# Kernel tuning notes

Measured on AMD Instinct MI355X. Metric: run time of the kernel, lower is better.

## Reference

```python
import jax, jax.numpy as jnp
import numpy as np

E, C, H, I = 8, 1024, 2048, 4096  # experts, capacity, hidden, intermediate


def setup_inputs() -> dict:
    key = jax.random.key(0)
    k1, k2, k3 = jax.random.split(key, 3)
    hidden_states = jax.random.normal(k1, (E, C, H), dtype=jnp.float32)
    # fused gate/up projection weights per expert: [E, H, 2*I]
    w_gate_up = jax.random.normal(k2, (E, H, 2 * I), dtype=jnp.float32) * (1.0 / np.sqrt(H))
    # down projection weights per expert: [E, I, H]
    w_down = jax.random.normal(k3, (E, I, H), dtype=jnp.float32) * (1.0 / np.sqrt(I))
    return {"hidden_states": hidden_states, "w_gate_up": w_gate_up, "w_down": w_down}


def reference(hidden_states, w_gate_up, w_down):
    # Batched per-expert gate/up GEMM: (E,C,H) @ (E,H,2I) -> (E,C,2I)
    gate_up = jnp.einsum("ech,ehf->ecf", hidden_states, w_gate_up)
    gate, up = jnp.split(gate_up, 2, axis=-1)  # each (E,C,I)
    act = jax.nn.silu(gate) * up  # GLU activation
    # Batched per-expert down GEMM: (E,C,I) @ (E,I,H) -> (E,C,H)
    out = jnp.einsum("eci,eih->ech", act, w_down)
    return out
```

## Files before the change

### kernel.cpp

```cpp
#include <hip/hip_runtime.h>
#include <stdint.h>


#define E_  8
#define C_  1024
#define H_  2048
#define I_  4096
#define N1_ 8192

typedef __bf16 bf16x8 __attribute__((ext_vector_type(8)));
typedef float  f32x4  __attribute__((ext_vector_type(4)));

typedef __attribute__((address_space(3))) unsigned       lds_uint;
typedef const __attribute__((address_space(1))) unsigned glob_uint;

__device__ __forceinline__ void gload_lds16(const void* g, void* l) {
    __builtin_amdgcn_global_load_lds((glob_uint*)g, (lds_uint*)l, 16, 0, 0);
}

__device__ __forceinline__ unsigned short f2bf(float f) {
    union { float f; unsigned u; } v; v.f = f;
    unsigned u = v.u;
    return (unsigned short)((u + 0x7FFFu + ((u >> 16) & 1u)) >> 16);
}

__device__ __forceinline__ unsigned swz8(unsigned row) {
    return ((row ^ (row >> 2)) & 7u) << 4;
}

#define SBAR0 __builtin_amdgcn_sched_barrier(0)
#define MFMA_ __builtin_amdgcn_mfma_f32_16x16x32_bf16

__global__ void k_convert(const float* __restrict__ src,
                          unsigned short* __restrict__ dst, int n8) {
    int idx = blockIdx.x * blockDim.x + threadIdx.x;
    int stride = gridDim.x * blockDim.x;
    for (int i = idx; i < n8; i += stride) {
        const float4* s = reinterpret_cast<const float4*>(src + (size_t)i * 8);
        float4 a = s[0], b = s[1];
        ushort4 lo, hi;
        lo.x = f2bf(a.x); lo.y = f2bf(a.y); lo.z = f2bf(a.z); lo.w = f2bf(a.w);
        hi.x = f2bf(b.x); hi.y = f2bf(b.y); hi.z = f2bf(b.z); hi.w = f2bf(b.w);
        ushort4* d = reinterpret_cast<ushort4*>(dst + (size_t)i * 8);
        d[0] = lo; d[1] = hi;
    }
}

template<int LD>
__device__ __forceinline__ void stageA(const char* __restrict__ gtile,
                                       char* ldst, int j, int tid, int wave) {
    unsigned p   = (unsigned)(j * 8192 + tid * 16);
    unsigned row = p >> 7;
    unsigned kb  = (p & 127u) ^ swz8(row);
    const char* gp = gtile + (size_t)row * LD + kb;
    void* lp = ldst + j * 8192 + wave * 1024;
    gload_lds16(gp, lp);
}

__device__ __forceinline__ const bf16x8* frag128(const char* tile, int row, int kb) {
    unsigned phys = (unsigned)(row * 128) + ((unsigned)kb ^ swz8((unsigned)row));
    return reinterpret_cast<const bf16x8*>(tile + phys);
}

template<int LDB>
__device__ __forceinline__ void loadB8(const char* __restrict__ gcol, int kt,
                                       float4 (&bk)[8]) {
    const char* p = gcol + (size_t)(kt * 64) * LDB;
    #pragma unroll
    for (int i = 0; i < 8; ++i)
        bk[i] = *reinterpret_cast<const float4*>(p + (size_t)i * LDB);
}

__device__ __forceinline__ void cvtWriteB(char* bB, const float4 (&bk)[8],
                                          int rg, int kg8) {
    const float* f = reinterpret_cast<const float*>(&bk[0]);
    #pragma unroll
    for (int j = 0; j < 4; ++j) {
        unsigned u[4];
        #pragma unroll
        for (int p2 = 0; p2 < 4; ++p2) {
            float lo = f[(2 * p2) * 4 + j];
            float hi = f[(2 * p2 + 1) * 4 + j];
            asm("v_cvt_pk_bf16_f32 %0, %1, %2" : "=v"(u[p2]) : "v"(lo), "v"(hi));
        }
        unsigned q = (unsigned)(rg * 4 + j);
        unsigned phys = q * 128 + (((unsigned)kg8 * 16) ^ swz8(q));
        *reinterpret_cast<uint4*>(bB + phys) = make_uint4(u[0], u[1], u[2], u[3]);
    }
}

template<int LDA, int LDB, int NT, int BMG, int BNG, int MODE>
__global__ __launch_bounds__(512, 2) void k_gemm_f(
    const unsigned short* __restrict__ A,
    const float* __restrict__ B,
    void* __restrict__ Cout,
    size_t sA, size_t sB) {
    __shared__ char lds[131072];

    const int tid = threadIdx.x, lane = tid & 63, wave = tid >> 6;
    const int wm = wave >> 2, wn = wave & 3;
    const int kg = lane >> 4, r = lane & 15;
    const int rg = tid & 63, kg8 = tid >> 6;

    unsigned flat = blockIdx.x;
    unsigned cpx = gridDim.x >> 3;
    unsigned nid = (flat & 7u) * cpx + (flat >> 3);
    const int bm = nid % BMG;
    const int bn = (nid / BMG) % BNG;
    const int e  = nid / (BMG * BNG);

    const char* gA = (const char*)(A + sA * e) + (size_t)(bm * 256) * LDA;
    size_t colstart;
    if constexpr (MODE == 0)
        colstart = (size_t)(bn * 128 + ((rg >> 4) & 3) * 32 + ((rg >> 2) & 1) * 16
                            + (rg & 3) * 4)
                 + (((rg >> 3) & 1) ? (size_t)I_ : (size_t)0);
    else
        colstart = (size_t)(bn * 256 + rg * 4);
    const char* gBcol = (const char*)B + sB * e + colstart * 4
                      + (size_t)kg8 * 8 * LDB;

    float4 bk[8];

    loadB8<LDB>(gBcol, 0, bk);
    SBAR0;
    asm volatile("s_waitcnt vmcnt(0)" ::: "memory");
    SBAR0;
    cvtWriteB(lds + 32768, bk, rg, kg8);
    SBAR0;
    stageA<LDA>(gA, lds, 0, tid, wave);
    stageA<LDA>(gA, lds, 1, tid, wave);
    stageA<LDA>(gA, lds, 2, tid, wave);
    stageA<LDA>(gA, lds, 3, tid, wave);
    SBAR0;
    loadB8<LDB>(gBcol, 1, bk);
    SBAR0;
    asm volatile("s_waitcnt vmcnt(8)" ::: "memory");
    asm volatile("s_waitcnt lgkmcnt(0)" ::: "memory");
    SBAR0;
    __builtin_amdgcn_s_barrier();
    SBAR0;

    f32x4 acc[8][4] = {};

    for (int t = 0; t < NT; ++t) {
        const char* Ab = lds + (t & 1) * 65536;
        const char* Bb = Ab + 32768;
        char* nA = lds + ((t + 1) & 1) * 65536;
        char* nB = nA + 32768;
        const char* gAn = gA + (size_t)(t + 1) * 128;
        const bool hs1 = (t + 1) < NT, hs2 = (t + 2) < NT;

        bf16x8 af[8], b0[2], bg[2];

        if (hs1) {
            asm volatile("s_waitcnt vmcnt(0)" ::: "memory");
            SBAR0;
            cvtWriteB(nB, bk, rg, kg8);
            SBAR0;
            stageA<LDA>(gAn, nA, 0, tid, wave);
            stageA<LDA>(gAn, nA, 1, tid, wave);
            stageA<LDA>(gAn, nA, 2, tid, wave);
            stageA<LDA>(gAn, nA, 3, tid, wave);
            SBAR0;
            if (hs2) { loadB8<LDB>(gBcol, t + 2, bk); SBAR0; }
        }

        #pragma unroll
        for (int m = 0; m < 8; ++m)
            af[m] = *frag128(Ab, wm * 128 + m * 16 + r, kg * 16);
        #pragma unroll
        for (int n = 0; n < 2; ++n)
            b0[n] = *frag128(Bb, wn * 64 + n * 16 + r, kg * 16);
        __builtin_amdgcn_s_setprio(1);
        #pragma unroll
        for (int m = 0; m < 8; ++m) {
            acc[m][0] = MFMA_(af[m], b0[0], acc[m][0], 0, 0, 0);
            acc[m][1] = MFMA_(af[m], b0[1], acc[m][1], 0, 0, 0);
        }
        __builtin_amdgcn_s_setprio(0);

        #pragma unroll
        for (int n = 0; n < 2; ++n)
            bg[n] = *frag128(Bb, wn * 64 + 32 + n * 16 + r, kg * 16);
        __builtin_amdgcn_s_setprio(1);
        #pragma unroll
        for (int m = 0; m < 8; ++m) {
            acc[m][2] = MFMA_(af[m], bg[0], acc[m][2], 0, 0, 0);
            acc[m][3] = MFMA_(af[m], bg[1], acc[m][3], 0, 0, 0);
        }
        __builtin_amdgcn_s_setprio(0);

        #pragma unroll
        for (int m = 0; m < 8; ++m)
            af[m] = *frag128(Ab, wm * 128 + m * 16 + r, 64 + kg * 16);
        #pragma unroll
        for (int n = 0; n < 2; ++n)
            b0[n] = *frag128(Bb, wn * 64 + n * 16 + r, 64 + kg * 16);
        __builtin_amdgcn_s_setprio(1);
        #pragma unroll
        for (int m = 0; m < 8; ++m) {
            acc[m][0] = MFMA_(af[m], b0[0], acc[m][0], 0, 0, 0);
            acc[m][1] = MFMA_(af[m], b0[1], acc[m][1], 0, 0, 0);
        }
        __builtin_amdgcn_s_setprio(0);

        #pragma unroll
        for (int n = 0; n < 2; ++n)
            bg[n] = *frag128(Bb, wn * 64 + 32 + n * 16 + r, 64 + kg * 16);
        __builtin_amdgcn_s_setprio(1);
        #pragma unroll
        for (int m = 0; m < 8; ++m) {
            acc[m][2] = MFMA_(af[m], bg[0], acc[m][2], 0, 0, 0);
            acc[m][3] = MFMA_(af[m], bg[1], acc[m][3], 0, 0, 0);
        }
        __builtin_amdgcn_s_setprio(0);

        if (hs1) {
            SBAR0;
            if (hs2) asm volatile("s_waitcnt vmcnt(8)" ::: "memory");
            else     asm volatile("s_waitcnt vmcnt(0)" ::: "memory");
            asm volatile("s_waitcnt lgkmcnt(0)" ::: "memory");
            SBAR0;
            __builtin_amdgcn_s_barrier();
            SBAR0;
        }
    }

    const int row0 = bm * 256 + wm * 128 + kg * 4;
    if constexpr (MODE == 0) {
        unsigned short* act = (unsigned short*)Cout + (size_t)e * C_ * I_;
        const int col0 = bn * 128 + wn * 32 + r;
        #pragma unroll
        for (int m = 0; m < 8; ++m)
            #pragma unroll
            for (int n = 0; n < 2; ++n)
                #pragma unroll
                for (int j = 0; j < 4; ++j) {
                    float g = acc[m][n][j], u = acc[m][n + 2][j];
                    float s = g / (1.0f + __expf(-g)) * u;
                    act[(size_t)(row0 + m * 16 + j) * I_ + col0 + n * 16] = f2bf(s);
                }
    } else {
        float* o = (float*)Cout + (size_t)e * C_ * H_;
        const int col0 = bn * 256 + wn * 64 + r;
        #pragma unroll
        for (int m = 0; m < 8; ++m)
            #pragma unroll
            for (int n = 0; n < 4; ++n)
                #pragma unroll
                for (int j = 0; j < 4; ++j)
                    o[(size_t)(row0 + m * 16 + j) * H_ + col0 + n * 16] = acc[m][n][j];
    }
}

extern "C" void kernel_launch(void* const* d_in, const int* in_sizes, int n_in,
                              void* d_out, int out_size, void* d_ws, size_t ws_size,
                              hipStream_t stream) {
    const float* hs  = (const float*)d_in[0];
    const float* wgu = (const float*)d_in[1];
    const float* wd  = (const float*)d_in[2];
    float* out = (float*)d_out;

    char* ws = (char*)d_ws;
    unsigned short* Xbf  = (unsigned short*)(ws);
    unsigned short* actb = (unsigned short*)(ws + 33554432ull);

    k_convert<<<2048, 256, 0, stream>>>(hs, Xbf, E_ * C_ * H_ / 8);

    k_gemm_f<H_ * 2, N1_ * 4, H_ / 64, 4, 32, 0><<<dim3(1024), 512, 0, stream>>>(
        Xbf, wgu, actb, (size_t)C_ * H_, (size_t)H_ * N1_ * 4);

    k_gemm_f<I_ * 2, H_ * 4, I_ / 64, 4, 8, 1><<<dim3(256), 512, 0, stream>>>(
        actb, wd, out, (size_t)C_ * I_, (size_t)I_ * H_ * 4);
}
```

Baseline: 470.7 us.

## Use 1024-thread blocks with 4x4 per-wave MFMA tiles and new LDS swizzle

Doubles the workgroup to 16 waves over the same 256x128/256x256 block tile, so each wave computes a 64x64 sub-tile (4x4 MFMAs) instead of 128x64. The B loader now fetches float2 per thread and writes two rows, and the LDS XOR swizzle gains an extra term. The aim is more waves to hide latency and fewer registers per thread, at the cost of more LDS fragment reads per MFMA and heavier barrier synchronisation. The launch_bounds(1024,4) request is unlikely to be met with 128KB of LDS per block.

New measurement: 788.8 us. 1.68x slower.

```diff
diff --git a/kernel.cpp b/kernel.cpp
--- a/kernel.cpp
+++ b/kernel.cpp
@@ -24,8 +24,8 @@
     return (unsigned short)((u + 0x7FFFu + ((u >> 16) & 1u)) >> 16);
 }
 
-__device__ __forceinline__ unsigned swz8(unsigned row) {
-    return ((row ^ (row >> 2)) & 7u) << 4;
+__device__ __forceinline__ unsigned swzf(unsigned q) {
+    return ((q ^ (q >> 1) ^ (q >> 2)) & 7u) << 4;
 }
 
 #define SBAR0 __builtin_amdgcn_sched_barrier(0)
@@ -49,48 +49,47 @@
 template<int LD>
 __device__ __forceinline__ void stageA(const char* __restrict__ gtile,
                                        char* ldst, int j, int tid, int wave) {
-    unsigned p   = (unsigned)(j * 8192 + tid * 16);
+    unsigned p   = (unsigned)(j * 16384 + tid * 16);
     unsigned row = p >> 7;
-    unsigned kb  = (p & 127u) ^ swz8(row);
+    unsigned kb  = (p & 127u) ^ swzf(row);
     const char* gp = gtile + (size_t)row * LD + kb;
-    void* lp = ldst + j * 8192 + wave * 1024;
+    void* lp = ldst + j * 16384 + wave * 1024;
     gload_lds16(gp, lp);
 }
 
 __device__ __forceinline__ const bf16x8* frag128(const char* tile, int row, int kb) {
-    unsigned phys = (unsigned)(row * 128) + ((unsigned)kb ^ swz8((unsigned)row));
+    unsigned phys = (unsigned)(row * 128) + ((unsigned)kb ^ swzf((unsigned)row));
     return reinterpret_cast<const bf16x8*>(tile + phys);
 }
 
 template<int LDB>
-__device__ __forceinline__ void loadB8(const char* __restrict__ gcol, int kt,
-                                       float4 (&bk)[8]) {
-    const char* p = gcol + (size_t)(kt * 64) * LDB;
+__device__ __forceinline__ void loadB8(const float* __restrict__ gcol, int kt,
+                                       float2 (&bk)[8]) {
+    const float* p = gcol + (size_t)(kt * 64) * LDB;
     #pragma unroll
     for (int i = 0; i < 8; ++i)
-        bk[i] = *reinterpret_cast<const float4*>(p + (size_t)i * LDB);
-}
-
-__device__ __forceinline__ void cvtWriteB(char* bB, const float4 (&bk)[8],
-                                          int rg, int kg8) {
-    const float* f = reinterpret_cast<const float*>(&bk[0]);
+        bk[i] = *reinterpret_cast<const float2*>(p + (size_t)i * LDB);
+}
+
+__device__ __forceinline__ void cvtWriteB(char* bB, const float2 (&bk)[8],
+                                          int rg, int ko) {
     #pragma unroll
-    for (int j = 0; j < 4; ++j) {
+    for (int cc = 0; cc < 2; ++cc) {
         unsigned u[4];
         #pragma unroll
         for (int p2 = 0; p2 < 4; ++p2) {
-            float lo = f[(2 * p2) * 4 + j];
-            float hi = f[(2 * p2 + 1) * 4 + j];
+            float lo = cc ? bk[2 * p2].y     : bk[2 * p2].x;
+            float hi = cc ? bk[2 * p2 + 1].y : bk[2 * p2 + 1].x;
             asm("v_cvt_pk_bf16_f32 %0, %1, %2" : "=v"(u[p2]) : "v"(lo), "v"(hi));
         }
-        unsigned q = (unsigned)(rg * 4 + j);
-        unsigned phys = q * 128 + (((unsigned)kg8 * 16) ^ swz8(q));
+        unsigned q = (unsigned)(2 * rg + cc);
+        unsigned phys = q * 128 + (((unsigned)ko * 16) ^ swzf(q));
         *reinterpret_cast<uint4*>(bB + phys) = make_uint4(u[0], u[1], u[2], u[3]);
     }
 }
 
 template<int LDA, int LDB, int NT, int BMG, int BNG, int MODE>
-__global__ __launch_bounds__(512, 2) void k_gemm_f(
+__global__ __launch_bounds__(1024, 4) void k_gemm_f(
     const unsigned short* __restrict__ A,
     const float* __restrict__ B,
     void* __restrict__ Cout,
@@ -100,7 +99,7 @@
     const int tid = threadIdx.x, lane = tid & 63, wave = tid >> 6;
     const int wm = wave >> 2, wn = wave & 3;
     const int kg = lane >> 4, r = lane & 15;
-    const int rg = tid & 63, kg8 = tid >> 6;
+    const int rg = tid & 127, ko = tid >> 7;
 
     unsigned flat = blockIdx.x;
     unsigned cpx = gridDim.x >> 3;
@@ -112,26 +111,22 @@
     const char* gA = (const char*)(A + sA * e) + (size_t)(bm * 256) * LDA;
     size_t colstart;
     if constexpr (MODE == 0)
-        colstart = (size_t)(bn * 128 + ((rg >> 4) & 3) * 32 + ((rg >> 2) & 1) * 16
-                            + (rg & 3) * 4)
+        colstart = (size_t)(bn * 128 + ((rg >> 4) * 16) + 2 * (rg & 7))
                  + (((rg >> 3) & 1) ? (size_t)I_ : (size_t)0);
     else
-        colstart = (size_t)(bn * 256 + rg * 4);
-    const char* gBcol = (const char*)B + sB * e + colstart * 4
-                      + (size_t)kg8 * 8 * LDB;
-
-    float4 bk[8];
+        colstart = (size_t)(bn * 256 + 2 * rg);
+    const float* gBcol = B + sB * e + colstart + (size_t)ko * 8 * LDB;
+
+    float2 bk[8];
 
     loadB8<LDB>(gBcol, 0, bk);
     SBAR0;
     asm volatile("s_waitcnt vmcnt(0)" ::: "memory");
     SBAR0;
-    cvtWriteB(lds + 32768, bk, rg, kg8);
+    cvtWriteB(lds + 32768, bk, rg, ko);
     SBAR0;
     stageA<LDA>(gA, lds, 0, tid, wave);
     stageA<LDA>(gA, lds, 1, tid, wave);
-    stageA<LDA>(gA, lds, 2, tid, wave);
-    stageA<LDA>(gA, lds, 3, tid, wave);
     SBAR0;
     loadB8<LDB>(gBcol, 1, bk);
     SBAR0;
@@ -141,7 +136,7 @@
     __builtin_amdgcn_s_barrier();
     SBAR0;
 
-    f32x4 acc[8][4] = {};
+    f32x4 acc[4][4] = {};
 
     for (int t = 0; t < NT; ++t) {
         const char* Ab = lds + (t & 1) * 65536;
@@ -151,70 +146,34 @@
         const char* gAn = gA + (size_t)(t + 1) * 128;
         const bool hs1 = (t + 1) < NT, hs2 = (t + 2) < NT;
 
-        bf16x8 af[8], b0[2], bg[2];
-
         if (hs1) {
             asm volatile("s_waitcnt vmcnt(0)" ::: "memory");
             SBAR0;
-            cvtWriteB(nB, bk, rg, kg8);
+            cvtWriteB(nB, bk, rg, ko);
             SBAR0;
             stageA<LDA>(gAn, nA, 0, tid, wave);
             stageA<LDA>(gAn, nA, 1, tid, wave);
-            stageA<LDA>(gAn, nA, 2, tid, wave);
-            stageA<LDA>(gAn, nA, 3, tid, wave);
             SBAR0;
             if (hs2) { loadB8<LDB>(gBcol, t + 2, bk); SBAR0; }
         }
 
         #pragma unroll
-        for (int m = 0; m < 8; ++m)
-            af[m] = *frag128(Ab, wm * 128 + m * 16 + r, kg * 16);
-        #pragma unroll
-        for (int n = 0; n < 2; ++n)
-            b0[n] = *frag128(Bb, wn * 64 + n * 16 + r, kg * 16);
-        __builtin_amdgcn_s_setprio(1);
-        #pragma unroll
-        for (int m = 0; m < 8; ++m) {
-            acc[m][0] = MFMA_(af[m], b0[0], acc[m][0], 0, 0, 0);
-            acc[m][1] = MFMA_(af[m], b0[1], acc[m][1], 0, 0, 0);
-        }
-        __builtin_amdgcn_s_setprio(0);
-
-        #pragma unroll
-        for (int n = 0; n < 2; ++n)
-            bg[n] = *frag128(Bb, wn * 64 + 32 + n * 16 + r, kg * 16);
-        __builtin_amdgcn_s_setprio(1);
-        #pragma unroll
-        for (int m = 0; m < 8; ++m) {
-            acc[m][2] = MFMA_(af[m], bg[0], acc[m][2], 0, 0, 0);
-            acc[m][3] = MFMA_(af[m], bg[1], acc[m][3], 0, 0, 0);
-        }
-        __builtin_amdgcn_s_setprio(0);
-
-        #pragma unroll
-        for (int m = 0; m < 8; ++m)
-            af[m] = *frag128(Ab, wm * 128 + m * 16 + r, 64 + kg * 16);
-        #pragma unroll
-        for (int n = 0; n < 2; ++n)
-            b0[n] = *frag128(Bb, wn * 64 + n * 16 + r, 64 + kg * 16);
-        __builtin_amdgcn_s_setprio(1);
-        #pragma unroll
-        for (int m = 0; m < 8; ++m) {
-            acc[m][0] = MFMA_(af[m], b0[0], acc[m][0], 0, 0, 0);
-            acc[m][1] = MFMA_(af[m], b0[1], acc[m][1], 0, 0, 0);
-        }
-        __builtin_amdgcn_s_setprio(0);
-
-        #pragma unroll
-        for (int n = 0; n < 2; ++n)
-            bg[n] = *frag128(Bb, wn * 64 + 32 + n * 16 + r, 64 + kg * 16);
-        __builtin_amdgcn_s_setprio(1);
-        #pragma unroll
-        for (int m = 0; m < 8; ++m) {
-            acc[m][2] = MFMA_(af[m], bg[0], acc[m][2], 0, 0, 0);
-            acc[m][3] = MFMA_(af[m], bg[1], acc[m][3], 0, 0, 0);
-        }
-        __builtin_amdgcn_s_setprio(0);
+        for (int kk = 0; kk < 2; ++kk) {
+            bf16x8 af[4], bf[4];
+            #pragma unroll
+            for (int m = 0; m < 4; ++m)
+                af[m] = *frag128(Ab, wm * 64 + m * 16 + r, kk * 64 + kg * 16);
+            #pragma unroll
+            for (int n = 0; n < 4; ++n)
+                bf[n] = *frag128(Bb, wn * 64 + n * 16 + r, kk * 64 + kg * 16);
+            __builtin_amdgcn_s_setprio(1);
+            #pragma unroll
+            for (int m = 0; m < 4; ++m)
+                #pragma unroll
+                for (int n = 0; n < 4; ++n)
+                    acc[m][n] = MFMA_(af[m], bf[n], acc[m][n], 0, 0, 0);
+            __builtin_amdgcn_s_setprio(0);
+        }
 
         if (hs1) {
             SBAR0;
@@ -227,25 +186,25 @@
         }
     }
 
-    const int row0 = bm * 256 + wm * 128 + kg * 4;
+    const int row0 = bm * 256 + wm * 64 + kg * 4;
     if constexpr (MODE == 0) {
         unsigned short* act = (unsigned short*)Cout + (size_t)e * C_ * I_;
         const int col0 = bn * 128 + wn * 32 + r;
         #pragma unroll
-        for (int m = 0; m < 8; ++m)
-            #pragma unroll
-            for (int n = 0; n < 2; ++n)
+        for (int m = 0; m < 4; ++m)
+            #pragma unroll
+            for (int p = 0; p < 2; ++p)
                 #pragma unroll
                 for (int j = 0; j < 4; ++j) {
-                    float g = acc[m][n][j], u = acc[m][n + 2][j];
+                    float g = acc[m][2 * p][j], u = acc[m][2 * p + 1][j];
                     float s = g / (1.0f + __expf(-g)) * u;
-                    act[(size_t)(row0 + m * 16 + j) * I_ + col0 + n * 16] = f2bf(s);
+                    act[(size_t)(row0 + m * 16 + j) * I_ + col0 + p * 16] = f2bf(s);
                 }
     } else {
         float* o = (float*)Cout + (size_t)e * C_ * H_;
         const int col0 = bn * 256 + wn * 64 + r;
         #pragma unroll
-        for (int m = 0; m < 8; ++m)
+        for (int m = 0; m < 4; ++m)
             #pragma unroll
             for (int n = 0; n < 4; ++n)
                 #pragma unroll
@@ -268,9 +227,9 @@
 
     k_convert<<<2048, 256, 0, stream>>>(hs, Xbf, E_ * C_ * H_ / 8);
 
-    k_gemm_f<H_ * 2, N1_ * 4, H_ / 64, 4, 32, 0><<<dim3(1024), 512, 0, stream>>>(
-        Xbf, wgu, actb, (size_t)C_ * H_, (size_t)H_ * N1_ * 4);
-
-    k_gemm_f<I_ * 2, H_ * 4, I_ / 64, 4, 8, 1><<<dim3(256), 512, 0, stream>>>(
-        actb, wd, out, (size_t)C_ * I_, (size_t)I_ * H_ * 4);
-}
+    k_gemm_f<H_ * 2, N1_, H_ / 64, 4, 32, 0><<<dim3(1024), 1024, 0, stream>>>(
+        Xbf, wgu, actb, (size_t)C_ * H_, (size_t)H_ * N1_);
+
+    k_gemm_f<I_ * 2, H_, I_ / 64, 4, 8, 1><<<dim3(256), 1024, 0, stream>>>(
+        actb, wd, out, (size_t)C_ * I_, (size_t)I_ * H_);
+}
```
